# Kernel tuning notes

Measured on AMD Instinct MI355X. Metric: run time of the kernel, lower is better.

Reference implementation:

```python
import jax, jax.numpy as jnp
import numpy as np

GROUP_SIZE = 128
N_BITS = 4
QMAX = 2 ** N_BITS - 1
NUM_EXPERTS = 8
HIDDEN = 2048
INTER = 768
NUM_ROT = 4
T_TOKENS = 4096
TOP_K = 2


def _make_pairs(rng, n_rot, in_feat):
    # intra-group permutation per rotation (valid disjoint Givens pairs)
    n_groups = in_feat // GROUP_SIZE
    return np.stack([
        np.concatenate([rng.permutation(GROUP_SIZE) for _ in range(n_groups)])
        for _ in range(n_rot)
    ]).astype(np.int32)


def _round_ste(x):
    return x + jax.lax.stop_gradient(jnp.round(x) - x)


def _rotate(W, pairs, angles):
    # W: [N, in_feat]; pairs: [R, in_feat] intra-group perm; angles: [R, in_feat//2]
    in_feat = W.shape[1]
    base = (jnp.arange(in_feat) // GROUP_SIZE) * GROUP_SIZE
    for r in range(pairs.shape[0]):
        abs_idx = base + pairs[r]
        i_idx = abs_idx[0::2]
        j_idx = abs_idx[1::2]
        c = jnp.cos(angles[r])
        s = jnp.sin(angles[r])
        wi = W[:, i_idx]
        wj = W[:, j_idx]
        W = W.at[:, i_idx].set(c * wi - s * wj).at[:, j_idx].set(s * wi + c * wj)
    return W


def _fake_quant(W):
    # groupwise asymmetric min-max fake quantization with STE rounding
    shape = W.shape
    wg = W.reshape(-1, GROUP_SIZE)
    wmax = wg.max(axis=-1, keepdims=True)
    wmin = wg.min(axis=-1, keepdims=True)
    scale = jnp.clip(wmax - wmin, 1e-5, None) / QMAX
    zero = jnp.round(-wmin / scale)
    q = jnp.clip(_round_ste(wg / scale) + zero, 0.0, float(QMAX))
    return ((q - zero) * scale).reshape(shape)


def _pseudo_quantize(W3, pairs, angles, ch_scales):
    # scale -> rotate -> fake-quant -> inverse rotate (reversed order, -angles) -> unscale
    E, O, In = W3.shape
    W = W3.reshape(-1, In) * ch_scales
    W = _rotate(W, pairs, angles)
    W = _fake_quant(W)
    W = _rotate(W, pairs[::-1], -angles[::-1])
    return (W / ch_scales).reshape(E, O, In)


def setup_inputs() -> dict:
    key = jax.random.key(0)
    ks = jax.random.split(key, 8)
    rng = np.random.default_rng(0)
    hidden_states = jax.random.normal(ks[0], (T_TOKENS, HIDDEN), jnp.float32)
    top_k_index = jax.random.randint(ks[1], (T_TOKENS, TOP_K), 0, NUM_EXPERTS, jnp.int32)
    logits = jax.random.normal(ks[2], (T_TOKENS, TOP_K), jnp.float32)
    top_k_weights = jax.nn.softmax(logits, axis=-1)
    gate_up_weight = jax.random.normal(ks[3], (NUM_EXPERTS, 2 * INTER, HIDDEN), jnp.float32) * 0.02
    down_weight = jax.random.normal(ks[4], (NUM_EXPERTS, HIDDEN, INTER), jnp.float32) * 0.02
    gate_up_pairs = jnp.asarray(_make_pairs(rng, NUM_ROT, HIDDEN))
    down_pairs = jnp.asarray(_make_pairs(rng, NUM_ROT, INTER))
    gate_up_angles = jax.random.normal(ks[5], (NUM_ROT, HIDDEN // 2), jnp.float32) * 0.1
    down_angles = jax.random.normal(ks[6], (NUM_ROT, INTER // 2), jnp.float32) * 0.1
    k7, k8 = jax.random.split(ks[7])
    gate_up_channel_scales = jax.random.uniform(k7, (1, HIDDEN), jnp.float32, 0.5, 1.5)
    down_channel_scales = jax.random.uniform(k8, (1, INTER), jnp.float32, 0.5, 1.5)
    return {
        "hidden_states": hidden_states,
        "top_k_index": top_k_index,
        "top_k_weights": top_k_weights,
        "gate_up_weight": gate_up_weight,
        "down_weight": down_weight,
        "gate_up_pairs": gate_up_pairs,
        "gate_up_angles": gate_up_angles,
        "down_pairs": down_pairs,
        "down_angles": down_angles,
        "gate_up_channel_scales": gate_up_channel_scales,
        "down_channel_scales": down_channel_scales,
    }


def reference(hidden_states, top_k_index, top_k_weights, gate_up_weight, down_weight,
              gate_up_pairs, gate_up_angles, down_pairs, down_angles,
              gate_up_channel_scales, down_channel_scales):
    # dequantize expert weights
    gup = _pseudo_quantize(gate_up_weight, gate_up_pairs, gate_up_angles, gate_up_channel_scales)  # [E,2I,H]
    dwn = _pseudo_quantize(down_weight, down_pairs, down_angles, down_channel_scales)              # [E,H,I]
    T = hidden_states.shape[0]
    E = gup.shape[0]
    # dense dispatch: all experts for all tokens (E small), combined by routing weights
    h = jnp.einsum('th,eoh->teo', hidden_states, gup)          # [T,E,2I]
    gate, up = jnp.split(h, 2, axis=-1)
    inter = jax.nn.silu(gate) * up                              # [T,E,I]
    y = jnp.einsum('tei,ehi->teh', inter, dwn)                  # [T,E,H]
    combine = jnp.zeros((T, E), hidden_states.dtype)
    combine = combine.at[jnp.arange(T)[:, None], top_k_index].add(top_k_weights)
    return jnp.einsum('teh,te->th', y, combine)
```

## Files before the change

### kernel.cpp

```cpp
#include <hip/hip_runtime.h>

#define T_TOKENS 4096
#define HIDDEN   2048
#define INTERM   768
#define NE       8
#define NPAIR    8192
#define NROT     4
#define MAXT     72

typedef __bf16 bf16x8 __attribute__((ext_vector_type(8)));
typedef float  f32x4  __attribute__((ext_vector_type(4)));

__device__ __forceinline__ unsigned short f2bf(float f) {
  unsigned u = __float_as_uint(f);
  u += 0x7fffu + ((u >> 16) & 1u);
  return (unsigned short)(u >> 16);
}

__device__ __forceinline__ void async16(const void* g, void* l) {
  __builtin_amdgcn_global_load_lds((const __attribute__((address_space(1))) void*)g,
                                   (__attribute__((address_space(3))) void*)l, 16, 0, 0);
}

__global__ void k_hist(const int* __restrict__ idx, int* __restrict__ cnt) {
  const int t = blockIdx.x * 256 + threadIdx.x;
  if (t < NPAIR) atomicAdd(&cnt[idx[t]], 1);
}

__global__ void k_scan(const int* __restrict__ cnt, int* __restrict__ off,
                       int* __restrict__ cur, int* __restrict__ tmap,
                       int* __restrict__ nv) {
  if (threadIdx.x == 0) {
    int a = 0, tt = 0;
    for (int e = 0; e < NE; ++e) {
      off[e] = a; cur[e] = 0;
      const int c = cnt[e];
      for (int m = 0; m < c; m += 128) tmap[tt++] = (e << 16) | (m >> 7);
      a += c;
    }
    nv[0] = tt;
    for (; tt < MAXT; ++tt) tmap[tt] = -1;
  }
}

__global__ void k_scatter(const int* __restrict__ idx, const float* __restrict__ wts,
                          const int* __restrict__ off, int* __restrict__ cur,
                          int* __restrict__ pt, float* __restrict__ pw) {
  const int t = blockIdx.x * 256 + threadIdx.x;
  if (t < NPAIR) {
    const int e = idx[t];
    const int pos = off[e] + atomicAdd(&cur[e], 1);
    pt[pos] = t;
    pw[pos] = wts[t];
  }
}

__global__ void k_tbl(const int* __restrict__ gp, const float* __restrict__ ga,
                      const int* __restrict__ dp, const float* __restrict__ da,
                      const float* __restrict__ gch, const float* __restrict__ dch,
                      float4* __restrict__ tg, float4* __restrict__ td,
                      float* __restrict__ grch, float* __restrict__ drch) {
  const int t = blockIdx.x * 256 + threadIdx.x;
  if (t < NROT * (HIDDEN / 2)) {
    const int r = t >> 10, s = t & 1023;
    const int grp = s >> 6;
    const int i = gp[r * HIDDEN + 2 * s], j = gp[r * HIDDEN + 2 * s + 1];
    const float a = ga[r * (HIDDEN / 2) + s];
    const float c = cosf(a), sn = sinf(a);
    tg[(grp * NROT + r) * 128 + i] = make_float4(c, -sn, __int_as_float(j), 0.f);
    tg[(grp * NROT + r) * 128 + j] = make_float4(c,  sn, __int_as_float(i), 0.f);
  }
  if (t < NROT * (INTERM / 2)) {
    const int r = t / (INTERM / 2), s = t - r * (INTERM / 2);
    const int grp = s >> 6;
    const int i = dp[r * INTERM + 2 * s], j = dp[r * INTERM + 2 * s + 1];
    const float a = da[r * (INTERM / 2) + s];
    const float c = cosf(a), sn = sinf(a);
    td[(grp * NROT + r) * 128 + i] = make_float4(c, -sn, __int_as_float(j), 0.f);
    td[(grp * NROT + r) * 128 + j] = make_float4(c,  sn, __int_as_float(i), 0.f);
  }
  if (t < HIDDEN) grch[t] = 1.0f / gch[t];
  if (t < INTERM) drch[t] = 1.0f / dch[t];
}

#define FWD_ROT(tl, v0, v1)                                                     \
  _Pragma("unroll")                                                             \
  for (int r = 0; r < NROT; ++r) {                                              \
    const float4 e0 = tl[r * 128 + l];                                          \
    const float4 e1 = tl[r * 128 + 64 + l];                                     \
    const int p0 = __float_as_int(e0.z), p1 = __float_as_int(e1.z);             \
    const int a0 = (p0 & 63) << 2, a1 = (p1 & 63) << 2;                         \
    _Pragma("unroll")                                                           \
    for (int q = 0; q < 4; ++q) {                                               \
      const int x0 = __float_as_int(v0[q]), x1 = __float_as_int(v1[q]);         \
      const float lo0 = __int_as_float(__builtin_amdgcn_ds_bpermute(a0, x0));   \
      const float hi0 = __int_as_float(__builtin_amdgcn_ds_bpermute(a0, x1));   \
      const float lo1 = __int_as_float(__builtin_amdgcn_ds_bpermute(a1, x0));   \
      const float hi1 = __int_as_float(__builtin_amdgcn_ds_bpermute(a1, x1));   \
      const float op0 = (p0 & 64) ? hi0 : lo0;                                  \
      const float op1 = (p1 & 64) ? hi1 : lo1;                                  \
      {                                                                         \
        _Pragma("clang fp contract(off)")                                       \
        v0[q] = e0.x * v0[q] + e0.y * op0;                                      \
        v1[q] = e1.x * v1[q] + e1.y * op1;                                      \
      }                                                                         \
    }                                                                           \
  }

__global__ __launch_bounds__(256) void k_quant(
    const float* __restrict__ W, const float4* __restrict__ tbl,
    const float* __restrict__ ch, unsigned short* __restrict__ out, int In, int G) {
  __shared__ float4 tl[NROT * 128];
  const int wv = threadIdx.x >> 6, l = threadIdx.x & 63;
  const int g = blockIdx.x % G;
  const int rowblk = blockIdx.x / G;
  const int row0 = rowblk * 16 + wv * 4;
  const int colbase = g << 7;
  tl[threadIdx.x]       = tbl[(size_t)g * NROT * 128 + threadIdx.x];
  tl[256 + threadIdx.x] = tbl[(size_t)g * NROT * 128 + 256 + threadIdx.x];
  __syncthreads();
  const float c0 = ch[colbase + l], c1 = ch[colbase + 64 + l];
  float v0[4], v1[4];
#pragma unroll
  for (int q = 0; q < 4; ++q) {
#pragma clang fp contract(off)
    const float* Wr = W + (size_t)(row0 + q) * In + colbase;
    v0[q] = Wr[l] * c0;
    v1[q] = Wr[64 + l] * c1;
  }
  FWD_ROT(tl, v0, v1)
#pragma unroll
  for (int q = 0; q < 4; ++q) {
    float mn = fminf(v0[q], v1[q]), mx = fmaxf(v0[q], v1[q]);
#pragma unroll
    for (int o = 32; o > 0; o >>= 1) {
      mn = fminf(mn, __shfl_xor(mn, o));
      mx = fmaxf(mx, __shfl_xor(mx, o));
    }
    {
#pragma clang fp contract(off)
      const float scale = fmaxf(mx - mn, 1e-5f) / 15.0f;
      const float zero = rintf(-mn / scale);
      const float q0 = fminf(fmaxf(rintf(v0[q] / scale) + zero, 0.0f), 15.0f);
      const float q1 = fminf(fmaxf(rintf(v1[q] / scale) + zero, 0.0f), 15.0f);
      v0[q] = (q0 - zero) * scale;
      v1[q] = (q1 - zero) * scale;
    }
  }
#pragma unroll
  for (int q = 0; q < 4; ++q) {
    unsigned short* Or = out + (size_t)(row0 + q) * In + colbase;
    Or[l]      = f2bf(v0[q]);
    Or[64 + l] = f2bf(v1[q]);
  }
}

__global__ __launch_bounds__(256) void k_rotx(
    const float* __restrict__ X, const float* __restrict__ rch,
    const float4* __restrict__ tbl, unsigned short* __restrict__ out) {
  __shared__ float4 tl[NROT * 128];
  const int wv = threadIdx.x >> 6, l = threadIdx.x & 63;
  const int g = blockIdx.x % 16;
  const int rowblk = blockIdx.x / 16;
  const int row0 = rowblk * 16 + wv * 4;
  const int colbase = g << 7;
  tl[threadIdx.x]       = tbl[(size_t)g * NROT * 128 + threadIdx.x];
  tl[256 + threadIdx.x] = tbl[(size_t)g * NROT * 128 + 256 + threadIdx.x];
  __syncthreads();
  const float i0 = rch[colbase + l], i1 = rch[colbase + 64 + l];
  float v0[4], v1[4];
#pragma unroll
  for (int q = 0; q < 4; ++q) {
    const float* Xr = X + (size_t)(row0 + q) * HIDDEN + colbase;
    v0[q] = Xr[l] * i0;
    v1[q] = Xr[64 + l] * i1;
  }
  FWD_ROT(tl, v0, v1)
#pragma unroll
  for (int q = 0; q < 4; ++q) {
    unsigned short* Or = out + (size_t)(row0 + q) * HIDDEN + colbase;
    Or[l]      = f2bf(v0[q]);
    Or[64 + l] = f2bf(v1[q]);
  }
}

__global__ __launch_bounds__(256) void k_silu2(
    const float* __restrict__ h, const float* __restrict__ pw,
    const float* __restrict__ rch, const float4* __restrict__ tbl,
    unsigned short* __restrict__ out) {
  __shared__ float4 tl[NROT * 128];
  const int wv = threadIdx.x >> 6, l = threadIdx.x & 63;
  const int g = blockIdx.x % 6;
  const int rowblk = blockIdx.x / 6;
  const int row0 = rowblk * 16 + wv * 4;
  const int colbase = g << 7;
  tl[threadIdx.x]       = tbl[(size_t)g * NROT * 128 + threadIdx.x];
  tl[256 + threadIdx.x] = tbl[(size_t)g * NROT * 128 + 256 + threadIdx.x];
  __syncthreads();
  const float i0 = rch[colbase + l], i1 = rch[colbase + 64 + l];
  float v0[4], v1[4];
#pragma unroll
  for (int q = 0; q < 4; ++q) {
    const int row = row0 + q;
    const float wgt = pw[row];
    const float* hr = h + (size_t)row * 1536 + colbase;
    const float g0 = hr[l], g1 = hr[64 + l];
    const float u0 = hr[768 + l], u1 = hr[768 + 64 + l];
    v0[q] = g0 / (1.0f + expf(-g0)) * u0 * wgt * i0;
    v1[q] = g1 / (1.0f + expf(-g1)) * u1 * wgt * i1;
  }
  FWD_ROT(tl, v0, v1)
#pragma unroll
  for (int q = 0; q < 4; ++q) {
    unsigned short* Or = out + (size_t)(row0 + q) * INTERM + colbase;
    Or[l]      = f2bf(v0[q]);
    Or[64 + l] = f2bf(v1[q]);
  }
}

template <int MODE>
__launch_bounds__(256, 4)
__global__ void k_gemm(const unsigned short* __restrict__ A,
                       const unsigned short* __restrict__ Bw,
                       float* __restrict__ C,
                       const int* __restrict__ pt,
                       const int* __restrict__ off,
                       const int* __restrict__ cnt,
                       const int* __restrict__ tmap,
                       const int* __restrict__ nv) {
  constexpr int K = MODE ? INTERM : HIDDEN;
  constexpr int N = MODE ? HIDDEN : 2 * INTERM;
  constexpr int XW = MODE ? 16 : 12;

  const int hw  = blockIdx.x + XW * blockIdx.y;
  const int xcd = hw & 7;
  const int pos = hw >> 3;
  const int nvalid = nv[0];
  const int q8 = nvalid >> 3, r8 = nvalid & 7;
  const int rs = q8 + (xcd < r8 ? 1 : 0);
  const int y0 = xcd * q8 + (xcd < r8 ? xcd : r8);
  if (pos >= rs * XW) return;
  int xg, yg;
  if (MODE == 1) {
    xg = pos & 15; yg = y0 + (pos >> 4);
  } else {
    const int cap6 = rs * 6;
    const int half = (pos >= cap6) ? 1 : 0;
    const int rem  = pos - half * cap6;
    xg = half * 6 + rem % 6;
    yg = y0 + rem / 6;
  }
  const int tm = tmap[yg];
  if (tm < 0) return;
  const int e = tm >> 16;
  const int m0 = (tm & 0xffff) << 7;
  const int count = cnt[e];
  const int seg = off[e];
  const int n0 = xg * 128;
  const unsigned short* Be = Bw + (size_t)e * N * K;

  __shared__ unsigned short As[2][128 * 32];
  __shared__ unsigned short Bs[2][128 * 32];

  const int tid = threadIdx.x;
  const int w = tid >> 6;
  const int l = tid & 63;
  const int r0 = w * 16 + (l >> 2);
  const int r1 = r0 + 64;
  const int kco = (l & 3) * 8;

  int p0 = m0 + r0; if (p0 > count - 1) p0 = count - 1;
  int p1 = m0 + r1; if (p1 > count - 1) p1 = count - 1;
  size_t arow0, arow1;
  if (MODE == 0) { arow0 = (size_t)(pt[seg + p0] >> 1); arow1 = (size_t)(pt[seg + p1] >> 1); }
  else           { arow0 = (size_t)(seg + p0); arow1 = (size_t)(seg + p1); }
  const unsigned short* pa0 = A + arow0 * K + kco;
  const unsigned short* pa1 = A + arow1 * K + kco;
  const unsigned short* pb0 = Be + (size_t)(n0 + r0) * K + kco;
  const unsigned short* pb1 = Be + (size_t)(n0 + r1) * K + kco;

  const int ko = (l >> 4) * 8;
  const int mrow = (w & 1) * 64 + (l & 15);
  const int nrow = (w >> 1) * 64 + (l & 15);

  f32x4 acc[4][4];
#pragma unroll
  for (int i = 0; i < 4; ++i)
#pragma unroll
    for (int j = 0; j < 4; ++j) acc[i][j] = (f32x4)0.0f;

  {
    async16(pa0, &As[0][w * 512]);
    async16(pa1, &As[0][(w + 4) * 512]);
    async16(pb0, &Bs[0][w * 512]);
    async16(pb1, &Bs[0][(w + 4) * 512]);
  }
  int buf = 0;
  for (int k0 = 0; k0 < K; k0 += 32, buf ^= 1) {
    __syncthreads();
    if (k0 + 32 < K) {
      const int kn = k0 + 32;
      async16(pa0 + kn, &As[buf ^ 1][w * 512]);
      async16(pa1 + kn, &As[buf ^ 1][(w + 4) * 512]);
      async16(pb0 + kn, &Bs[buf ^ 1][w * 512]);
      async16(pb1 + kn, &Bs[buf ^ 1][(w + 4) * 512]);
    }
    bf16x8 af[4], bfr[4];
#pragma unroll
    for (int i = 0; i < 4; ++i)
      af[i] = *(const bf16x8*)&As[buf][(mrow + i * 16) * 32 + ko];
#pragma unroll
    for (int j = 0; j < 4; ++j)
      bfr[j] = *(const bf16x8*)&Bs[buf][(nrow + j * 16) * 32 + ko];
#pragma unroll
    for (int i = 0; i < 4; ++i)
#pragma unroll
      for (int j = 0; j < 4; ++j)
        acc[i][j] = __builtin_amdgcn_mfma_f32_16x16x32_bf16(af[i], bfr[j], acc[i][j], 0, 0, 0);
  }

  const int mb = (w & 1) * 64 + (l >> 4) * 4;
  const int nb = n0 + (w >> 1) * 64 + (l & 15);
#pragma unroll
  for (int i = 0; i < 4; ++i) {
#pragma unroll
    for (int j = 0; j < 4; ++j) {
#pragma unroll
      for (int r = 0; r < 4; ++r) {
        const int mm = m0 + mb + i * 16 + r;
        if (mm < count) {
          const int nn = nb + j * 16;
          if (MODE == 0) {
            C[(size_t)(seg + mm) * N + nn] = acc[i][j][r];
          } else {
            C[(size_t)pt[seg + mm] * N + nn] = acc[i][j][r];
          }
        }
      }
    }
  }
}

__global__ __launch_bounds__(256) void k_combine(const float4* __restrict__ y,
                                                 float4* __restrict__ out) {
  const int t = blockIdx.x;
  const float4* y0 = y + (size_t)(2 * t) * (HIDDEN / 4);
  const float4* y1 = y + (size_t)(2 * t + 1) * (HIDDEN / 4);
  float4* o = out + (size_t)t * (HIDDEN / 4);
#pragma unroll
  for (int q = 0; q < 2; ++q) {
    const int c = threadIdx.x + q * 256;
    const float4 a = y0[c], b = y1[c];
    o[c] = make_float4(a.x + b.x, a.y + b.y, a.z + b.z, a.w + b.w);
  }
}

extern "C" void kernel_launch(void* const* d_in, const int* in_sizes, int n_in,
                              void* d_out, int out_size, void* d_ws, size_t ws_size,
                              hipStream_t stream) {
  const float* hs  = (const float*)d_in[0];
  const int*   tki = (const int*)d_in[1];
  const float* tkw = (const float*)d_in[2];
  const float* guw = (const float*)d_in[3];
  const float* dww = (const float*)d_in[4];
  const int*   gupr= (const int*)d_in[5];
  const float* gua = (const float*)d_in[6];
  const int*   dwp = (const int*)d_in[7];
  const float* dwa = (const float*)d_in[8];
  const float* gus = (const float*)d_in[9];
  const float* dwsc= (const float*)d_in[10];
  float* out = (float*)d_out;
  char* ws = (char*)d_ws;

  unsigned short* gup_bf = (unsigned short*)(ws + 0);
  unsigned short* dwn_bf = (unsigned short*)(ws + 50331648);
  unsigned short* x_bf   = (unsigned short*)(ws + 75497472);
  float*          hbuf   = (float*)(ws + 92274688);
  unsigned short* interb = (unsigned short*)(ws + 142606336);
  float*          ybuf   = (float*)(ws + 75497472);
  int*            pt     = (int*)(ws + 155189248);
  float*          pw     = (float*)(ws + 155222016);
  int*            cnt    = (int*)(ws + 155254784);
  int*            off    = cnt + 8;
  int*            cur    = cnt + 16;
  int*            tmap   = cnt + 24;
  int*            nv     = cnt + 120;
  float4*         tg     = (float4*)(ws + 155258880);
  float4*         td     = (float4*)(ws + 155389952);
  float*          grch   = (float*)(ws + 155439104);
  float*          drch   = (float*)(ws + 155447296);

  (void)hipMemsetAsync(cnt, 0, 32, stream);

  k_hist<<<32, 256, 0, stream>>>(tki, cnt);
  k_scan<<<1, 64, 0, stream>>>(cnt, off, cur, tmap, nv);
  k_scatter<<<32, 256, 0, stream>>>(tki, tkw, off, cur, pt, pw);
  k_tbl<<<16, 256, 0, stream>>>(gupr, gua, dwp, dwa, gus, dwsc, tg, td, grch, drch);
  k_rotx<<<4096, 256, 0, stream>>>(hs, grch, tg, x_bf);
  k_quant<<<12288, 256, 0, stream>>>(guw, tg, gus, gup_bf, HIDDEN, 16);
  k_quant<<<6144, 256, 0, stream>>>(dww, td, dwsc, dwn_bf, INTERM, 6);
  k_gemm<0><<<dim3(12, MAXT), 256, 0, stream>>>(x_bf, gup_bf, hbuf, pt, off, cnt, tmap, nv);
  k_silu2<<<3072, 256, 0, stream>>>(hbuf, pw, drch, td, interb);
  k_gemm<1><<<dim3(16, MAXT), 256, 0, stream>>>(interb, dwn_bf, ybuf, pt, off, cnt, tmap, nv);
  k_combine<<<T_TOKENS, 256, 0, stream>>>((const float4*)ybuf, (float4*)out);
}
```

Measured before the change: 536.3 us.

## Triple-buffer GEMM LDS tiles with explicit vmcnt waits for deeper prefetch

The grouped MoE GEMM moves from double to triple buffering in LDS. Loads are issued two k-steps ahead and guarded by manual s_waitcnt vmcnt/lgkmcnt plus a raw barrier, so one tile stays in flight while another is consumed. This is meant to hide more global-load latency behind MFMA work. In exchange LDS per block grows by half and launch bounds drop from 4 to 3 blocks per CU, which lowers occupancy.

```diff
diff --git a/kernel.cpp b/kernel.cpp
--- a/kernel.cpp
+++ b/kernel.cpp
@@ -219,7 +219,7 @@
 }
 
 template <int MODE>
-__launch_bounds__(256, 4)
+__launch_bounds__(256, 3)
 __global__ void k_gemm(const unsigned short* __restrict__ A,
                        const unsigned short* __restrict__ Bw,
                        float* __restrict__ C,
@@ -259,8 +259,8 @@
   const int n0 = xg * 128;
   const unsigned short* Be = Bw + (size_t)e * N * K;
 
-  __shared__ unsigned short As[2][128 * 32];
-  __shared__ unsigned short Bs[2][128 * 32];
+  __shared__ unsigned short As[3][128 * 32];
+  __shared__ unsigned short Bs[3][128 * 32];
 
   const int tid = threadIdx.x;
   const int w = tid >> 6;
@@ -289,21 +289,27 @@
 #pragma unroll
     for (int j = 0; j < 4; ++j) acc[i][j] = (f32x4)0.0f;
 
-  {
-    async16(pa0, &As[0][w * 512]);
-    async16(pa1, &As[0][(w + 4) * 512]);
-    async16(pb0, &Bs[0][w * 512]);
-    async16(pb1, &Bs[0][(w + 4) * 512]);
-  }
+#define STAGE(b, kn) do {                              \
+    async16(pa0 + (kn), &As[b][w * 512]);              \
+    async16(pa1 + (kn), &As[b][(w + 4) * 512]);        \
+    async16(pb0 + (kn), &Bs[b][w * 512]);              \
+    async16(pb1 + (kn), &Bs[b][(w + 4) * 512]);        \
+  } while (0)
+
+  STAGE(0, 0);
+  STAGE(1, 32);
+
   int buf = 0;
-  for (int k0 = 0; k0 < K; k0 += 32, buf ^= 1) {
-    __syncthreads();
-    if (k0 + 32 < K) {
-      const int kn = k0 + 32;
-      async16(pa0 + kn, &As[buf ^ 1][w * 512]);
-      async16(pa1 + kn, &As[buf ^ 1][(w + 4) * 512]);
-      async16(pb0 + kn, &Bs[buf ^ 1][w * 512]);
-      async16(pb1 + kn, &Bs[buf ^ 1][(w + 4) * 512]);
+  for (int k0 = 0; k0 < K; k0 += 32) {
+    asm volatile("s_waitcnt lgkmcnt(0)" ::: "memory");
+    if (k0 + 32 < K) asm volatile("s_waitcnt vmcnt(4)" ::: "memory");
+    else             asm volatile("s_waitcnt vmcnt(0)" ::: "memory");
+    __builtin_amdgcn_s_barrier();
+    __builtin_amdgcn_sched_barrier(0);
+    const int kn = k0 + 64;
+    if (kn < K) {
+      const int nb3 = (buf == 0) ? 2 : buf - 1;
+      STAGE(nb3, kn);
     }
     bf16x8 af[4], bfr[4];
 #pragma unroll
@@ -317,7 +323,9 @@
 #pragma unroll
       for (int j = 0; j < 4; ++j)
         acc[i][j] = __builtin_amdgcn_mfma_f32_16x16x32_bf16(af[i], bfr[j], acc[i][j], 0, 0, 0);
-  }
+    buf = (buf == 2) ? 0 : buf + 1;
+  }
+#undef STAGE
 
   const int mb = (w & 1) * 64 + (l >> 4) * 4;
   const int nb = n0 + (w >> 1) * 64 + (l & 15);
```

Measured after the change: 558.7 us. +4.2%, slower.
